# Kernel optimization log

Measured on AMD Instinct MI355X. Metric: run time of the kernel, lower is better.

## Reference

```python
import jax, jax.numpy as jnp
import numpy as np


def _lstm_layer(x, h0, c0, w_ih, w_hh, b):
    """x: [T,B,I], h0/c0: [B,H], w_ih: [4H,I], w_hh: [4H,H], b: [4H]. PyTorch gate order i,f,g,o."""
    H = h0.shape[-1]
    # Precompute input projection for all timesteps in one big GEMM.
    xg = jnp.einsum('tbi,gi->tbg', x, w_ih) + b  # [T,B,4H]

    def step(carry, xg_t):
        h, c = carry
        g = xg_t + h @ w_hh.T  # [B,4H]
        i, f, gg, o = jnp.split(g, 4, axis=-1)
        c_new = jax.nn.sigmoid(f) * c + jax.nn.sigmoid(i) * jnp.tanh(gg)
        h_new = jax.nn.sigmoid(o) * jnp.tanh(c_new)
        return (h_new, c_new), h_new

    (_, _), hs = jax.lax.scan(step, (h0, c0), xg)
    return hs  # [T,B,H]


def setup_inputs() -> dict:
    key = jax.random.key(0)
    ks = jax.random.split(key, 12)
    T, B, I, H, O, L = 2048, 32, 256, 512, 1024, 2
    s = 1.0 / np.sqrt(H)  # PyTorch LSTM init scale
    return {
        'x': jax.random.normal(ks[0], (T, B, I), jnp.float32),
        'h0': jnp.zeros((L, B, H), jnp.float32),
        'c0': jnp.zeros((L, B, H), jnp.float32),
        'w_ih0': jax.random.normal(ks[1], (4 * H, I), jnp.float32) * s,
        'w_hh0': jax.random.normal(ks[2], (4 * H, H), jnp.float32) * s,
        'b_ih0': jax.random.normal(ks[3], (4 * H,), jnp.float32) * s,
        'b_hh0': jax.random.normal(ks[4], (4 * H,), jnp.float32) * s,
        'w_ih1': jax.random.normal(ks[5], (4 * H, H), jnp.float32) * s,
        'w_hh1': jax.random.normal(ks[6], (4 * H, H), jnp.float32) * s,
        'b_ih1': jax.random.normal(ks[7], (4 * H,), jnp.float32) * s,
        'b_hh1': jax.random.normal(ks[8], (4 * H,), jnp.float32) * s,
        'fc_w': jax.random.normal(ks[9], (O, H), jnp.float32) * s,
        'fc_b': jax.random.normal(ks[10], (O,), jnp.float32) * s,
    }


def reference(x, h0, c0, w_ih0, w_hh0, b_ih0, b_hh0, w_ih1, w_hh1, b_ih1, b_hh1, fc_w, fc_b):
    h1 = _lstm_layer(x, h0[0], c0[0], w_ih0, w_hh0, b_ih0 + b_hh0)   # [T,B,H]
    h2 = _lstm_layer(h1, h0[1], c0[1], w_ih1, w_hh1, b_ih1 + b_hh1)  # [T,B,H]
    logits = h2[-1] @ fc_w.T + fc_b  # out[-1] -> fc, [B,O]
    return jax.nn.log_softmax(logits, axis=1)
```

## Files before the change

kernel.cpp:

```cpp
#include <hip/hip_runtime.h>
#include <stdint.h>

#define TT 2048
#define BB 32
#define II 256
#define HH 512
#define OO 1024
#define NWGL 16
#define NWG 32
#define RING 32
#define SLOTB (BB * HH * 2)

typedef __attribute__((ext_vector_type(8))) short short8;
typedef __attribute__((ext_vector_type(4))) float floatx4;

__device__ __forceinline__ unsigned short f2bf(float f) {
  union { float f; unsigned u; } v; v.f = f;
  unsigned r = v.u + 0x7FFFu + ((v.u >> 16) & 1u);
  return (unsigned short)(r >> 16);
}
__device__ __forceinline__ float bf2f(unsigned short b) {
  union { float f; unsigned u; } v; v.u = ((unsigned)b) << 16; return v.f;
}
__device__ __forceinline__ float sigmf(float x) { return 1.0f / (1.0f + __expf(-x)); }
__device__ __forceinline__ float tanhfast(float x) {
  float xc = fminf(fmaxf(x, -15.f), 15.f);
  float e = __expf(2.f * xc);
  return (e - 1.f) / (e + 1.f);
}

#define LD1(d, va, IMM)                                                     \
  asm volatile("global_load_dwordx4 %0, %1, off offset:" IMM " sc0 sc1"     \
               : "=v"(d) : "v"(va) : "memory")

#define ISSUE8KB(dst, va) do {                                              \
    unsigned long long _v1 = (va), _v2 = (va) + 4096;                       \
    LD1(dst[0], _v1, "0");    LD1(dst[1], _v1, "1024");                     \
    LD1(dst[2], _v1, "2048"); LD1(dst[3], _v1, "3072");                     \
    LD1(dst[4], _v2, "0");    LD1(dst[5], _v2, "1024");                     \
    LD1(dst[6], _v2, "2048"); LD1(dst[7], _v2, "3072"); } while (0)

#define WAITV(N) do {                                                       \
    asm volatile("s_waitcnt vmcnt(" #N ")" ::: "memory");                   \
    __builtin_amdgcn_sched_barrier(0); } while (0)

#define DSW8(buf, tile, w8) do {                                            \
    _Pragma("unroll")                                                       \
    for (int j = 0; j < 8; j++)                                             \
      *reinterpret_cast<short8*>(&(tile)[((w8) + j) * 512 + (lane ^ j) * 8]) = (buf)[j]; \
    } while (0)

#define LDSA(tile, b, kk)                                                   \
  (*reinterpret_cast<const short8*>(&(tile)[(b) * 512 + (((kk) * 4 + krow) ^ c7) * 8]))

#define PROGREAD(dst, addr64)                                               \
  asm volatile("global_load_dword %0, %1, off sc0 sc1"                      \
               : "=v"(dst) : "v"(addr64) : "memory")

#define SEQSTORE(arr, slot, val) do {                                       \
    if (lane == 0) {                                                        \
      unsigned long long _a = (unsigned long long)(arr) +                   \
          (unsigned long long)((slot) * 64 + g) * 4;                        \
      int _v = (val);                                                       \
      asm volatile("global_store_dword %0, %1, off sc0 sc1"                 \
                   :: "v"(_a), "v"(_v) : "memory");                         \
    } } while (0)

#define VALIDATE(arr, slot, tag) do {                                       \
    const unsigned long long _sa = (unsigned long long)(arr) +              \
        (unsigned long long)((slot) * 64 + lane) * 4;                       \
    int _sv; PROGREAD(_sv, _sa); WAITV(0);                                  \
    while (!__all(_sv == (tag))) {                                          \
      __builtin_amdgcn_s_sleep(1); PROGREAD(_sv, _sa); WAITV(0);            \
    } } while (0)

#define TAIL(hwaddr) do {                                                   \
  _Pragma("unroll")                                                         \
  for (int tau = 0; tau < 2; tau++) {                                       \
    _Pragma("unroll")                                                       \
    for (int tt = 0; tt < 2; tt++) {                                        \
      _Pragma("unroll")                                                     \
      for (int r = 0; r < 4; r++) {                                         \
        float val = acc[tau][tt][r];                                        \
        float nl = (gate == 2) ? tanhfast(val) : sigmf(val);                \
        int base2 = (lane & 48) | u;                                        \
        float iv = __shfl(nl, base2);                                       \
        float fv = __shfl(nl, base2 | 4);                                   \
        float gv = __shfl(nl, base2 | 8);                                   \
        float ov = __shfl(nl, base2 | 12);                                  \
        if (gate == 0) {                                                    \
          float cn = fv * cst[tau][tt][r] + iv * gv;                        \
          cst[tau][tt][r] = cn;                                             \
          float hn = ov * tanhfast(cn);                                     \
          int b = tt * 16 + krow * 4 + r;                                   \
          sh[w][b][tau * 4 + u] = f2bf(hn);                                 \
        }                                                                   \
      }                                                                     \
    }                                                                       \
  }                                                                         \
  asm volatile("s_waitcnt lgkmcnt(0)" ::: "memory");                        \
  __builtin_amdgcn_sched_barrier(0);                                        \
  if (lane < 32) {                                                          \
    short8 v = *reinterpret_cast<const short8*>(&sh[w][lane][0]);           \
    unsigned long long sa = (hwaddr) + stoff;                               \
    asm volatile("global_store_dwordx4 %0, %1, off sc0 sc1"                 \
                 :: "v"(sa), "v"(v) : "memory");                            \
  } } while (0)

__global__ void k_convert_x(const float* __restrict__ x, ushort* __restrict__ xb, int n4) {
  int i = blockIdx.x * blockDim.x + threadIdx.x;
  int stride = gridDim.x * blockDim.x;
  const float4* xf = reinterpret_cast<const float4*>(x);
  ushort4* ob = reinterpret_cast<ushort4*>(xb);
  for (; i < n4; i += stride) {
    float4 f = xf[i];
    ushort4 o;
    o.x = f2bf(f.x); o.y = f2bf(f.y); o.z = f2bf(f.z); o.w = f2bf(f.w);
    ob[i] = o;
  }
}

__global__ void k_init(const float* __restrict__ h0in,
                       ushort* __restrict__ h0ring, ushort* __restrict__ h1ring,
                       int* __restrict__ h0seq, int* __restrict__ h1seq,
                       int* __restrict__ pr1) {
  int i = threadIdx.x;
  ushort* s0 = h0ring + (RING - 1) * BB * HH;
  ushort* s1 = h1ring + (RING - 1) * BB * HH;
  for (int k = i; k < BB * HH; k += blockDim.x) {
    s0[k] = f2bf(h0in[k]);
    s1[k] = f2bf(h0in[BB * HH + k]);
  }
  for (int k = i; k < RING * 64; k += blockDim.x) {
    int v = (k >= (RING - 1) * 64) ? -1 : (int)0x80000000;
    h0seq[k] = v;
    h1seq[k] = v;
  }
  for (int k = i; k < 64; k += blockDim.x) pr1[k] = -1;
}

__global__ __launch_bounds__(256, 1) void k_lstm(
    const ushort* __restrict__ xb,
    const float* __restrict__ w_ih0, const float* __restrict__ w_hh0,
    const float* __restrict__ b_ih0, const float* __restrict__ b_hh0,
    const float* __restrict__ w_ih1, const float* __restrict__ w_hh1,
    const float* __restrict__ b_ih1, const float* __restrict__ b_hh1,
    const float* __restrict__ c0in,
    ushort* __restrict__ h0ring, ushort* __restrict__ h1ring,
    int* __restrict__ h0seq, int* __restrict__ h1seq,
    int* __restrict__ pr1)
{
  __shared__ ushort t0[32 * 512];
  __shared__ ushort t1[32 * 512];
  __shared__ ushort sh[4][BB][8];
  const int wg = blockIdx.x;
  const int tid = threadIdx.x;
  const int w = tid >> 6;
  const int lane = tid & 63;
  const bool isL0 = wg < NWGL;
  const int G = isL0 ? wg : wg - NWGL;
  const int g = G * 4 + w;
  const int col = lane & 15;
  const int krow = lane >> 4;
  const int u = col & 3;
  const int gate = col >> 2;
  const int c7 = col & 7;

  short8 wf[2][32];
#define LOADW(dst, base, rowlen, kbase, tau) do {                             \
    const int _grow = gate * HH + g * 8 + (tau) * 4 + u;                      \
    const float* _p = (base) + (size_t)_grow * (rowlen) + (kbase) + krow * 8; \
    short8 _r;                                                                \
    _Pragma("unroll")                                                         \
    for (int _j = 0; _j < 8; _j++) _r[_j] = (short)f2bf(_p[_j]);              \
    (dst) = _r; } while (0)

  if (isL0) {
#pragma unroll
    for (int tau = 0; tau < 2; tau++) {
#pragma unroll
      for (int kk = 0; kk < 8; kk++)  LOADW(wf[tau][kk],      w_ih0, II, kk * 32, tau);
#pragma unroll
      for (int kk = 0; kk < 16; kk++) LOADW(wf[tau][8 + kk],  w_hh0, HH, kk * 32, tau);
    }
  } else {
#pragma unroll
    for (int tau = 0; tau < 2; tau++) {
#pragma unroll
      for (int kk = 0; kk < 16; kk++) LOADW(wf[tau][kk],      w_ih1, HH, kk * 32, tau);
#pragma unroll
      for (int kk = 0; kk < 16; kk++) LOADW(wf[tau][16 + kk], w_hh1, HH, kk * 32, tau);
    }
  }
  float bias[2];
#pragma unroll
  for (int tau = 0; tau < 2; tau++) {
    const int grow = gate * HH + g * 8 + tau * 4 + u;
    bias[tau] = isL0 ? (b_ih0[grow] + b_hh0[grow]) : (b_ih1[grow] + b_hh1[grow]);
  }

  float cst[2][2][4];
  {
    const float* cbase = c0in + (isL0 ? 0 : 1) * BB * HH;
#pragma unroll
    for (int tau = 0; tau < 2; tau++)
#pragma unroll
      for (int tt = 0; tt < 2; tt++)
#pragma unroll
        for (int r = 0; r < 4; r++) {
          int b = tt * 16 + krow * 4 + r;
          cst[tau][tt][r] = cbase[b * HH + g * 8 + tau * 4 + u];
        }
  }

  const unsigned long long h0rb = (unsigned long long)h0ring;
  const unsigned long long h1rb = (unsigned long long)h1ring;
  const unsigned long long stoff = (unsigned long long)(lane * 1024 + g * 16);
  const unsigned long long stagevo = (unsigned long long)(w * 8192 + lane * 16);

  short8 wa[8], wb[8];
  floatx4 acc[2][2];
  const floatx4 bi0 = (floatx4){ bias[0], bias[0], bias[0], bias[0] };
  const floatx4 bi1 = (floatx4){ bias[1], bias[1], bias[1], bias[1] };

  if (isL0) {
    for (int t = 0; t < TT; ++t) {
      if (w == 0) {
        VALIDATE(h0seq, (t + 31) & 31, t - 1);
        if (((t & 7) == 0) && t >= 32) {
          const unsigned long long pa = (unsigned long long)pr1 + lane * 4ull;
          int pv; PROGREAD(pv, pa); WAITV(0);
          while (!__all(pv >= t - 24)) {
            __builtin_amdgcn_s_sleep(4); PROGREAD(pv, pa); WAITV(0);
          }
        }
      }
      __syncthreads();
      ISSUE8KB(wa, h0rb + (unsigned long long)((t + 31) & 31) * SLOTB + stagevo);
      WAITV(0);
      DSW8(wa, t0, w * 8);
      __syncthreads();
      acc[0][0] = bi0; acc[0][1] = bi0; acc[1][0] = bi1; acc[1][1] = bi1;
      const char* xr = (const char*)xb + (size_t)t * (BB * II * 2);
#pragma unroll
      for (int tt = 0; tt < 2; tt++) {
        const int b = tt * 16 + col;
#pragma unroll
        for (int kk = 0; kk < 8; kk++) {
          short8 a = *reinterpret_cast<const short8*>(xr + b * 512 + kk * 64 + krow * 16);
          acc[0][tt] = __builtin_amdgcn_mfma_f32_16x16x32_bf16(a, wf[0][kk], acc[0][tt], 0, 0, 0);
          acc[1][tt] = __builtin_amdgcn_mfma_f32_16x16x32_bf16(a, wf[1][kk], acc[1][tt], 0, 0, 0);
        }
#pragma unroll
        for (int kk = 0; kk < 16; kk++) {
          short8 a = LDSA(t0, b, kk);
          acc[0][tt] = __builtin_amdgcn_mfma_f32_16x16x32_bf16(a, wf[0][8 + kk], acc[0][tt], 0, 0, 0);
          acc[1][tt] = __builtin_amdgcn_mfma_f32_16x16x32_bf16(a, wf[1][8 + kk], acc[1][tt], 0, 0, 0);
        }
      }
      TAIL(h0rb + (unsigned long long)(t & 31) * SLOTB);
      WAITV(0);
      SEQSTORE(h0seq, (t & 31), t);
    }
  } else {
    for (int t = 0; t < TT; ++t) {
      if (w == 0) {
        const unsigned long long sa0 = (unsigned long long)h0seq +
            (unsigned long long)((t & 31) * 64 + lane) * 4;
        const unsigned long long sa1 = (unsigned long long)h1seq +
            (unsigned long long)(((t + 31) & 31) * 64 + lane) * 4;
        int s0, s1; PROGREAD(s0, sa0); PROGREAD(s1, sa1); WAITV(0);
        while (!(__all(s0 == t) & __all(s1 == t - 1))) {
          __builtin_amdgcn_s_sleep(1);
          PROGREAD(s0, sa0); PROGREAD(s1, sa1); WAITV(0);
        }
      }
      __syncthreads();
      ISSUE8KB(wa, h0rb + (unsigned long long)(t & 31) * SLOTB + stagevo);
      ISSUE8KB(wb, h1rb + (unsigned long long)((t + 31) & 31) * SLOTB + stagevo);
      WAITV(8);
      DSW8(wa, t0, w * 8);
      WAITV(0);
      DSW8(wb, t1, w * 8);
      if (lane == 0) {
        unsigned long long pa = (unsigned long long)pr1 + (unsigned long long)g * 4;
        int pv = t;
        asm volatile("global_store_dword %0, %1, off sc0 sc1"
                     :: "v"(pa), "v"(pv) : "memory");
      }
      __syncthreads();
      acc[0][0] = bi0; acc[0][1] = bi0; acc[1][0] = bi1; acc[1][1] = bi1;
#pragma unroll
      for (int tt = 0; tt < 2; tt++) {
        const int b = tt * 16 + col;
#pragma unroll
        for (int kk = 0; kk < 16; kk++) {
          short8 a = LDSA(t0, b, kk);
          acc[0][tt] = __builtin_amdgcn_mfma_f32_16x16x32_bf16(a, wf[0][kk], acc[0][tt], 0, 0, 0);
          acc[1][tt] = __builtin_amdgcn_mfma_f32_16x16x32_bf16(a, wf[1][kk], acc[1][tt], 0, 0, 0);
        }
#pragma unroll
        for (int kk = 0; kk < 16; kk++) {
          short8 a = LDSA(t1, b, kk);
          acc[0][tt] = __builtin_amdgcn_mfma_f32_16x16x32_bf16(a, wf[0][16 + kk], acc[0][tt], 0, 0, 0);
          acc[1][tt] = __builtin_amdgcn_mfma_f32_16x16x32_bf16(a, wf[1][16 + kk], acc[1][tt], 0, 0, 0);
        }
      }
      TAIL(h1rb + (unsigned long long)(t & 31) * SLOTB);
      WAITV(0);
      SEQSTORE(h1seq, (t & 31), t);
    }
  }
}

__global__ __launch_bounds__(256) void k_fc(const ushort* __restrict__ h1,
                                            const float* __restrict__ fcw,
                                            const float* __restrict__ fcb,
                                            float* __restrict__ out) {
  __shared__ float hsh[HH];
  __shared__ float red[256];
  const int b = blockIdx.x, tid = threadIdx.x;
  for (int k = tid; k < HH; k += 256) hsh[k] = bf2f(h1[b * HH + k]);
  __syncthreads();
  float lg[4];
#pragma unroll
  for (int q = 0; q < 4; q++) {
    int o = q * 256 + tid;
    float acc = fcb[o];
    const float* wr = fcw + (size_t)o * HH;
#pragma unroll 4
    for (int k = 0; k < HH; k += 4) {
      float4 w4 = *reinterpret_cast<const float4*>(wr + k);
      acc += hsh[k] * w4.x + hsh[k + 1] * w4.y + hsh[k + 2] * w4.z + hsh[k + 3] * w4.w;
    }
    lg[q] = acc;
  }
  float m = fmaxf(fmaxf(lg[0], lg[1]), fmaxf(lg[2], lg[3]));
  red[tid] = m; __syncthreads();
  for (int s = 128; s > 0; s >>= 1) { if (tid < s) red[tid] = fmaxf(red[tid], red[tid + s]); __syncthreads(); }
  m = red[0]; __syncthreads();
  float se = 0.f;
#pragma unroll
  for (int q = 0; q < 4; q++) se += __expf(lg[q] - m);
  red[tid] = se; __syncthreads();
  for (int s = 128; s > 0; s >>= 1) { if (tid < s) red[tid] += red[tid + s]; __syncthreads(); }
  float lse = m + logf(red[0]);
#pragma unroll
  for (int q = 0; q < 4; q++) out[b * OO + q * 256 + tid] = lg[q] - lse;
}

extern "C" void kernel_launch(void* const* d_in, const int* in_sizes, int n_in,
                              void* d_out, int out_size, void* d_ws, size_t ws_size,
                              hipStream_t stream) {
  const float* x     = (const float*)d_in[0];
  const float* h0    = (const float*)d_in[1];
  const float* c0    = (const float*)d_in[2];
  const float* w_ih0 = (const float*)d_in[3];
  const float* w_hh0 = (const float*)d_in[4];
  const float* b_ih0 = (const float*)d_in[5];
  const float* b_hh0 = (const float*)d_in[6];
  const float* w_ih1 = (const float*)d_in[7];
  const float* w_hh1 = (const float*)d_in[8];
  const float* b_ih1 = (const float*)d_in[9];
  const float* b_hh1 = (const float*)d_in[10];
  const float* fcw   = (const float*)d_in[11];
  const float* fcb   = (const float*)d_in[12];
  float* out = (float*)d_out;

  char* ws = (char*)d_ws;
  size_t off = 0;
  ushort* xb     = (ushort*)(ws + off); off += (size_t)TT * BB * II * 2;
  ushort* h0ring = (ushort*)(ws + off); off += (size_t)RING * BB * HH * 2;
  ushort* h1ring = (ushort*)(ws + off); off += (size_t)RING * BB * HH * 2;
  int* h0seq = (int*)(ws + off); off += RING * 64 * sizeof(int);
  int* h1seq = (int*)(ws + off); off += RING * 64 * sizeof(int);
  int* pr1   = (int*)(ws + off); off += 64 * sizeof(int);

  k_convert_x<<<2048, 256, 0, stream>>>(x, xb, TT * BB * II / 4);
  k_init<<<1, 256, 0, stream>>>(h0, h0ring, h1ring, h0seq, h1seq, pr1);
  k_lstm<<<NWG, 256, 0, stream>>>(xb, w_ih0, w_hh0, b_ih0, b_hh0,
                                  w_ih1, w_hh1, b_ih1, b_hh1, c0,
                                  h0ring, h1ring, h0seq, h1seq, pr1);
  k_fc<<<BB, 256, 0, stream>>>(h1ring + (RING - 1) * BB * HH, fcw, fcb, out);
}
```

Before: 18.02 ms.

## Use direct global-to-LDS loads and prefetch layer-0 h into double buffer

```diff
diff --git a/kernel.cpp b/kernel.cpp
--- a/kernel.cpp
+++ b/kernel.cpp
@@ -29,29 +29,24 @@
   return (e - 1.f) / (e + 1.f);
 }
 
-#define LD1(d, va, IMM)                                                     \
-  asm volatile("global_load_dwordx4 %0, %1, off offset:" IMM " sc0 sc1"     \
-               : "=v"(d) : "v"(va) : "memory")
-
-#define ISSUE8KB(dst, va) do {                                              \
-    unsigned long long _v1 = (va), _v2 = (va) + 4096;                       \
-    LD1(dst[0], _v1, "0");    LD1(dst[1], _v1, "1024");                     \
-    LD1(dst[2], _v1, "2048"); LD1(dst[3], _v1, "3072");                     \
-    LD1(dst[4], _v2, "0");    LD1(dst[5], _v2, "1024");                     \
-    LD1(dst[6], _v2, "2048"); LD1(dst[7], _v2, "3072"); } while (0)
-
 #define WAITV(N) do {                                                       \
     asm volatile("s_waitcnt vmcnt(" #N ")" ::: "memory");                   \
     __builtin_amdgcn_sched_barrier(0); } while (0)
 
-#define DSW8(buf, tile, w8) do {                                            \
+#define GLD8(tile, gslot) do {                                              \
     _Pragma("unroll")                                                       \
     for (int j = 0; j < 8; j++)                                             \
-      *reinterpret_cast<short8*>(&(tile)[((w8) + j) * 512 + (lane ^ j) * 8]) = (buf)[j]; \
+      __builtin_amdgcn_global_load_lds(                                     \
+        (const __attribute__((address_space(1))) void*)                     \
+          ((gslot) + (unsigned long long)((w8 + j) * 1024) +                \
+           (unsigned)(laneoff ^ (j << 4))),                                 \
+        (__attribute__((address_space(3))) void*)&(tile)[(w8 + j) * 512],   \
+        16, 0, 17);                                                         \
     } while (0)
 
 #define LDSA(tile, b, kk)                                                   \
-  (*reinterpret_cast<const short8*>(&(tile)[(b) * 512 + (((kk) * 4 + krow) ^ c7) * 8]))
+  (*reinterpret_cast<const short8*>(                                        \
+      &(tile)[(b) * 512 + ((((kk) * 32 + krow * 8) ^ (((b) & 7) << 3)))]))
 
 #define PROGREAD(dst, addr64)                                               \
   asm volatile("global_load_dword %0, %1, off sc0 sc1"                      \
@@ -64,14 +59,6 @@
       int _v = (val);                                                       \
       asm volatile("global_store_dword %0, %1, off sc0 sc1"                 \
                    :: "v"(_a), "v"(_v) : "memory");                         \
-    } } while (0)
-
-#define VALIDATE(arr, slot, tag) do {                                       \
-    const unsigned long long _sa = (unsigned long long)(arr) +              \
-        (unsigned long long)((slot) * 64 + lane) * 4;                       \
-    int _sv; PROGREAD(_sv, _sa); WAITV(0);                                  \
-    while (!__all(_sv == (tag))) {                                          \
-      __builtin_amdgcn_s_sleep(1); PROGREAD(_sv, _sa); WAITV(0);            \
     } } while (0)
 
 #define TAIL(hwaddr) do {                                                   \
@@ -150,8 +137,8 @@
     int* __restrict__ h0seq, int* __restrict__ h1seq,
     int* __restrict__ pr1)
 {
-  __shared__ ushort t0[32 * 512];
-  __shared__ ushort t1[32 * 512];
+  __shared__ ushort h0t[2][32 * 512];
+  __shared__ ushort h1t[32 * 512];
   __shared__ ushort sh[4][BB][8];
   const int wg = blockIdx.x;
   const int tid = threadIdx.x;
@@ -164,7 +151,8 @@
   const int krow = lane >> 4;
   const int u = col & 3;
   const int gate = col >> 2;
-  const int c7 = col & 7;
+  const int w8 = w * 8;
+  const int laneoff = lane * 16;
 
   short8 wf[2][32];
 #define LOADW(dst, base, rowlen, kbase, tau) do {                             \
@@ -216,9 +204,7 @@
   const unsigned long long h0rb = (unsigned long long)h0ring;
   const unsigned long long h1rb = (unsigned long long)h1ring;
   const unsigned long long stoff = (unsigned long long)(lane * 1024 + g * 16);
-  const unsigned long long stagevo = (unsigned long long)(w * 8192 + lane * 16);
-
-  short8 wa[8], wb[8];
+
   floatx4 acc[2][2];
   const floatx4 bi0 = (floatx4){ bias[0], bias[0], bias[0], bias[0] };
   const floatx4 bi1 = (floatx4){ bias[1], bias[1], bias[1], bias[1] };
@@ -226,7 +212,12 @@
   if (isL0) {
     for (int t = 0; t < TT; ++t) {
       if (w == 0) {
-        VALIDATE(h0seq, (t + 31) & 31, t - 1);
+        const unsigned long long sa = (unsigned long long)h0seq +
+            (unsigned long long)(((t + 31) & 31) * 64 + lane) * 4;
+        int sv; PROGREAD(sv, sa); WAITV(0);
+        while (!__all(sv == t - 1)) {
+          __builtin_amdgcn_s_sleep(1); PROGREAD(sv, sa); WAITV(0);
+        }
         if (((t & 7) == 0) && t >= 32) {
           const unsigned long long pa = (unsigned long long)pr1 + lane * 4ull;
           int pv; PROGREAD(pv, pa); WAITV(0);
@@ -236,10 +227,7 @@
         }
       }
       __syncthreads();
-      ISSUE8KB(wa, h0rb + (unsigned long long)((t + 31) & 31) * SLOTB + stagevo);
-      WAITV(0);
-      DSW8(wa, t0, w * 8);
-      __syncthreads();
+      GLD8(h0t[0], h0rb + (unsigned long long)((t + 31) & 31) * SLOTB);
       acc[0][0] = bi0; acc[0][1] = bi0; acc[1][0] = bi1; acc[1][1] = bi1;
       const char* xr = (const char*)xb + (size_t)t * (BB * II * 2);
 #pragma unroll
@@ -251,9 +239,15 @@
           acc[0][tt] = __builtin_amdgcn_mfma_f32_16x16x32_bf16(a, wf[0][kk], acc[0][tt], 0, 0, 0);
           acc[1][tt] = __builtin_amdgcn_mfma_f32_16x16x32_bf16(a, wf[1][kk], acc[1][tt], 0, 0, 0);
         }
+      }
+      WAITV(0);
+      __syncthreads();
+#pragma unroll
+      for (int tt = 0; tt < 2; tt++) {
+        const int b = tt * 16 + col;
 #pragma unroll
         for (int kk = 0; kk < 16; kk++) {
-          short8 a = LDSA(t0, b, kk);
+          short8 a = LDSA(h0t[0], b, kk);
           acc[0][tt] = __builtin_amdgcn_mfma_f32_16x16x32_bf16(a, wf[0][8 + kk], acc[0][tt], 0, 0, 0);
           acc[1][tt] = __builtin_amdgcn_mfma_f32_16x16x32_bf16(a, wf[1][8 + kk], acc[1][tt], 0, 0, 0);
         }
@@ -263,25 +257,69 @@
       SEQSTORE(h0seq, (t & 31), t);
     }
   } else {
+    int cur = 0;
+    if (w == 0) {
+      const unsigned long long sa = (unsigned long long)h0seq +
+          (unsigned long long)(0 * 64 + lane) * 4;
+      int sv; PROGREAD(sv, sa); WAITV(0);
+      while (!__all(sv == 0)) {
+        __builtin_amdgcn_s_sleep(1); PROGREAD(sv, sa); WAITV(0);
+      }
+    }
+    __syncthreads();
+    GLD8(h0t[0], h0rb);
+    WAITV(0);
+    __syncthreads();
+
     for (int t = 0; t < TT; ++t) {
+      const bool pf = (t < TT - 1);
       if (w == 0) {
-        const unsigned long long sa0 = (unsigned long long)h0seq +
-            (unsigned long long)((t & 31) * 64 + lane) * 4;
         const unsigned long long sa1 = (unsigned long long)h1seq +
             (unsigned long long)(((t + 31) & 31) * 64 + lane) * 4;
-        int s0, s1; PROGREAD(s0, sa0); PROGREAD(s1, sa1); WAITV(0);
-        while (!(__all(s0 == t) & __all(s1 == t - 1))) {
-          __builtin_amdgcn_s_sleep(1);
-          PROGREAD(s0, sa0); PROGREAD(s1, sa1); WAITV(0);
+        const unsigned long long sa0 = (unsigned long long)h0seq +
+            (unsigned long long)(((t + 1) & 31) * 64 + lane) * 4;
+        if (pf) {
+          int s1v, s0v; PROGREAD(s1v, sa1); PROGREAD(s0v, sa0); WAITV(0);
+          while (!(__all(s1v == t - 1) & __all(s0v == t + 1))) {
+            __builtin_amdgcn_s_sleep(1);
+            PROGREAD(s1v, sa1); PROGREAD(s0v, sa0); WAITV(0);
+          }
+        } else {
+          int s1v; PROGREAD(s1v, sa1); WAITV(0);
+          while (!__all(s1v == t - 1)) {
+            __builtin_amdgcn_s_sleep(1); PROGREAD(s1v, sa1); WAITV(0);
+          }
         }
       }
       __syncthreads();
-      ISSUE8KB(wa, h0rb + (unsigned long long)(t & 31) * SLOTB + stagevo);
-      ISSUE8KB(wb, h1rb + (unsigned long long)((t + 31) & 31) * SLOTB + stagevo);
-      WAITV(8);
-      DSW8(wa, t0, w * 8);
+      GLD8(h1t, h1rb + (unsigned long long)((t + 31) & 31) * SLOTB);
+      if (pf)
+        GLD8(h0t[cur ^ 1], h0rb + (unsigned long long)((t + 1) & 31) * SLOTB);
+      acc[0][0] = bi0; acc[0][1] = bi0; acc[1][0] = bi1; acc[1][1] = bi1;
+      if (cur == 0) {
+#pragma unroll
+        for (int tt = 0; tt < 2; tt++) {
+          const int b = tt * 16 + col;
+#pragma unroll
+          for (int kk = 0; kk < 16; kk++) {
+            short8 a = LDSA(h0t[0], b, kk);
+            acc[0][tt] = __builtin_amdgcn_mfma_f32_16x16x32_bf16(a, wf[0][kk], acc[0][tt], 0, 0, 0);
+            acc[1][tt] = __builtin_amdgcn_mfma_f32_16x16x32_bf16(a, wf[1][kk], acc[1][tt], 0, 0, 0);
+          }
+        }
+      } else {
+#pragma unroll
+        for (int tt = 0; tt < 2; tt++) {
+          const int b = tt * 16 + col;
+#pragma unroll
+          for (int kk = 0; kk < 16; kk++) {
+            short8 a = LDSA(h0t[1], b, kk);
+            acc[0][tt] = __builtin_amdgcn_mfma_f32_16x16x32_bf16(a, wf[0][kk], acc[0][tt], 0, 0, 0);
+            acc[1][tt] = __builtin_amdgcn_mfma_f32_16x16x32_bf16(a, wf[1][kk], acc[1][tt], 0, 0, 0);
+          }
+        }
+      }
       WAITV(0);
-      DSW8(wb, t1, w * 8);
       if (lane == 0) {
         unsigned long long pa = (unsigned long long)pr1 + (unsigned long long)g * 4;
         int pv = t;
@@ -289,19 +327,12 @@
                      :: "v"(pa), "v"(pv) : "memory");
       }
       __syncthreads();
-      acc[0][0] = bi0; acc[0][1] = bi0; acc[1][0] = bi1; acc[1][1] = bi1;
 #pragma unroll
       for (int tt = 0; tt < 2; tt++) {
         const int b = tt * 16 + col;
 #pragma unroll
         for (int kk = 0; kk < 16; kk++) {
-          short8 a = LDSA(t0, b, kk);
-          acc[0][tt] = __builtin_amdgcn_mfma_f32_16x16x32_bf16(a, wf[0][kk], acc[0][tt], 0, 0, 0);
-          acc[1][tt] = __builtin_amdgcn_mfma_f32_16x16x32_bf16(a, wf[1][kk], acc[1][tt], 0, 0, 0);
-        }
-#pragma unroll
-        for (int kk = 0; kk < 16; kk++) {
-          short8 a = LDSA(t1, b, kk);
+          short8 a = LDSA(h1t, b, kk);
           acc[0][tt] = __builtin_amdgcn_mfma_f32_16x16x32_bf16(a, wf[0][16 + kk], acc[0][tt], 0, 0, 0);
           acc[1][tt] = __builtin_amdgcn_mfma_f32_16x16x32_bf16(a, wf[1][16 + kk], acc[1][tt], 0, 0, 0);
         }
@@ -309,6 +340,7 @@
       TAIL(h1rb + (unsigned long long)(t & 31) * SLOTB);
       WAITV(0);
       SEQSTORE(h1seq, (t & 31), t);
+      cur ^= 1;
     }
   }
 }
```

Result: slower. 20.59 ms (+14.2%).
